# Performance work log

Hardware: AMD Instinct MI355X
Metric: run time of the kernel (lower is better)

Reference implementation:

```python
import jax, jax.numpy as jnp
import numpy as np

N = 10000          # num mesh vertices
NSPEC = 64         # spectral basis size (V[:, :64], D[:64, :])
K = 6              # Chebyshev order
IN_DESC = 352      # input descriptor dims (SHOT)
OUT_DESC = 256     # output descriptor dims
EPS = 1e-3


def _bn(x, g, b):
    # BatchNorm1d over the node (batch) dim, training-mode batch statistics
    m = x.mean(axis=0)
    v = x.var(axis=0)
    return (x - m) * jax.lax.rsqrt(v + EPS) * g + b


def _cheb(x, V, D, eigs, W, b):
    # Spectral Laplacian apply: L z = V @ (eigs * (D @ z)); cost O(N*64*C)
    def L(z):
        return V @ (eigs[:, None] * (D @ z))
    T_prev, T_cur = x, L(x)
    out = T_prev @ W[0] + T_cur @ W[1]
    for k in range(2, K):
        T_next = 2.0 * L(T_cur) - T_prev
        out = out + T_next @ W[k]
        T_prev, T_cur = T_cur, T_next
    return out + b


def setup_inputs() -> dict:
    key = jax.random.key(0)
    ks = jax.random.split(key, 12)
    s = lambda fan_in: 1.0 / np.sqrt(fan_in)
    return {
        "x": jax.random.normal(ks[0], (N, IN_DESC), jnp.float32),
        "V": jax.random.normal(ks[1], (N, NSPEC), jnp.float32) * (1.0 / np.sqrt(N)),
        "D": jax.random.normal(ks[2], (NSPEC, N), jnp.float32) * (1.0 / np.sqrt(N)),
        "eigs": jax.random.uniform(ks[3], (NSPEC,), jnp.float32),
        "fc1_w": jax.random.normal(ks[4], (IN_DESC, 64), jnp.float32) * s(IN_DESC),
        "fc1_b": jnp.zeros((64,), jnp.float32),
        "bf1_g": jnp.ones((64,), jnp.float32),
        "bf1_b": jnp.zeros((64,), jnp.float32),
        "W1": jax.random.normal(ks[5], (K, 64, 64), jnp.float32) * s(64 * K),
        "cb1": jnp.zeros((64,), jnp.float32),
        "b1_g": jnp.ones((64,), jnp.float32),
        "b1_b": jnp.zeros((64,), jnp.float32),
        "W2": jax.random.normal(ks[6], (K, 64, 64), jnp.float32) * s(64 * K),
        "cb2": jnp.zeros((64,), jnp.float32),
        "b2_g": jnp.ones((64,), jnp.float32),
        "b2_b": jnp.zeros((64,), jnp.float32),
        "W3": jax.random.normal(ks[7], (K, 64, 128), jnp.float32) * s(64 * K),
        "cb3": jnp.zeros((128,), jnp.float32),
        "b3_g": jnp.ones((128,), jnp.float32),
        "b3_b": jnp.zeros((128,), jnp.float32),
        "fc2_w": jax.random.normal(ks[8], (128, OUT_DESC), jnp.float32) * s(128),
        "fc2_b": jnp.zeros((OUT_DESC,), jnp.float32),
        "bf2_g": jnp.ones((OUT_DESC,), jnp.float32),
        "bf2_b": jnp.zeros((OUT_DESC,), jnp.float32),
        "fc3_w": jax.random.normal(ks[9], (OUT_DESC, N), jnp.float32) * s(OUT_DESC),
        "fc3_b": jnp.zeros((N,), jnp.float32),
    }


def reference(x, V, D, eigs, fc1_w, fc1_b, bf1_g, bf1_b,
              W1, cb1, b1_g, b1_b, W2, cb2, b2_g, b2_b,
              W3, cb3, b3_g, b3_b, fc2_w, fc2_b, bf2_g, bf2_b,
              fc3_w, fc3_b):
    h = jax.nn.relu(_bn(x @ fc1_w + fc1_b, bf1_g, bf1_b))
    h = jax.nn.relu(_bn(_cheb(h, V, D, eigs, W1, cb1), b1_g, b1_b))
    h = jax.nn.relu(_bn(_cheb(h, V, D, eigs, W2, cb2), b2_g, b2_b))
    h = jax.nn.relu(_bn(_cheb(h, V, D, eigs, W3, cb3), b3_g, b3_b))
    desc = jax.nn.relu(_bn(h @ fc2_w + fc2_b, bf2_g, bf2_b))
    logits = desc @ fc3_w + fc3_b  # [N, N] correspondence logits
    return jax.nn.log_softmax(logits, axis=1), desc
```

## Files before the change

kernel.cpp:

```cpp
#include <hip/hip_runtime.h>
#include <hip/hip_bf16.h>

#define NV 10000
#define PADM 10112

typedef __attribute__((ext_vector_type(8))) short bf16x8;
typedef __attribute__((ext_vector_type(4))) float f32x4;

__device__ __forceinline__ void g2l16(const void* g, void* l) {
  __builtin_amdgcn_global_load_lds((__attribute__((address_space(1))) void*)(void*)g,
                                   (__attribute__((address_space(3))) void*)l, 16, 0, 0);
}

__global__ __launch_bounds__(256) void gemm_f32(
    const float* __restrict__ A1, int K1, const float* __restrict__ A2, int K2,
    const float* __restrict__ B, const float* __restrict__ bias,
    float* __restrict__ Y, float* __restrict__ stats, int N)
{
  __shared__ float As[64][36];
  __shared__ float Bs[32][68];
  const int tid = threadIdx.x;
  const int row0 = blockIdx.x * 64;
  const int n0 = blockIdx.y * 64;
  const int tr = tid >> 4, tc = tid & 15;
  const int Ktot = K1 + K2;
  float acc[4][4];
#pragma unroll
  for (int i = 0; i < 4; ++i)
#pragma unroll
    for (int j = 0; j < 4; ++j) acc[i][j] = 0.f;

  for (int k0 = 0; k0 < Ktot; k0 += 32) {
    const float* Ap; int lda, ka;
    if (k0 < K1) { Ap = A1; lda = K1; ka = k0; }
    else         { Ap = A2; lda = K2; ka = k0 - K1; }
    __syncthreads();
    {
      int r = tid >> 3, seg = tid & 7;
#pragma unroll
      for (int h = 0; h < 2; ++h) {
        int rr = r + h * 32;
        int gr = row0 + rr; if (gr > NV - 1) gr = NV - 1;
        float4 v = *(const float4*)(Ap + (size_t)gr * lda + ka + seg * 4);
        *(float4*)&As[rr][seg * 4] = v;
      }
      int kr = tid >> 4, cseg = tid & 15;
#pragma unroll
      for (int h = 0; h < 2; ++h) {
        int kk = kr + h * 16;
        float4 v = *(const float4*)(B + (size_t)(k0 + kk) * N + n0 + cseg * 4);
        *(float4*)&Bs[kk][cseg * 4] = v;
      }
    }
    __syncthreads();
#pragma unroll 8
    for (int kk = 0; kk < 32; ++kk) {
      float4 bv = *(const float4*)&Bs[kk][tc * 4];
#pragma unroll
      for (int i = 0; i < 4; ++i) {
        float a = As[tr * 4 + i][kk];
        acc[i][0] = fmaf(a, bv.x, acc[i][0]);
        acc[i][1] = fmaf(a, bv.y, acc[i][1]);
        acc[i][2] = fmaf(a, bv.z, acc[i][2]);
        acc[i][3] = fmaf(a, bv.w, acc[i][3]);
      }
    }
  }
  float bvv[4];
#pragma unroll
  for (int j = 0; j < 4; ++j) bvv[j] = bias[n0 + tc * 4 + j];
  float cs[4] = {0.f, 0.f, 0.f, 0.f}, cq[4] = {0.f, 0.f, 0.f, 0.f};
#pragma unroll
  for (int i = 0; i < 4; ++i) {
    int gr = row0 + tr * 4 + i;
    bool ok = gr < NV;
    float o[4];
#pragma unroll
    for (int j = 0; j < 4; ++j) {
      float v = acc[i][j] + bvv[j];
      o[j] = v;
      if (ok) { cs[j] += v; cq[j] += v * v; }
    }
    if (ok) *(float4*)(Y + (size_t)gr * N + n0 + tc * 4) = make_float4(o[0], o[1], o[2], o[3]);
  }
  __syncthreads();
  float* red = &As[0][0];
#pragma unroll
  for (int j = 0; j < 4; ++j) {
    red[tr * 68 + tc * 4 + j] = cs[j];
    red[1088 + tr * 68 + tc * 4 + j] = cq[j];
  }
  __syncthreads();
  if (tid < 64) {
    float s = 0.f, q = 0.f;
#pragma unroll
    for (int t = 0; t < 16; ++t) { s += red[t * 68 + tid]; q += red[1088 + t * 68 + tid]; }
    atomicAdd(&stats[n0 + tid], s);
    atomicAdd(&stats[256 + n0 + tid], q);
  }
}

__global__ __launch_bounds__(256) void bn_relu(
    const float* __restrict__ Y, const float* __restrict__ stats,
    const float* __restrict__ g, const float* __restrict__ bt,
    float* __restrict__ out, unsigned short* __restrict__ outb, int C)
{
  int gid = blockIdx.x * 256 + threadIdx.x;
  int total = NV * (C >> 2);
  if (gid >= total) return;
  int c = (gid * 4) % C;
  float4 y = *(const float4*)(Y + (size_t)gid * 4);
  float vy[4] = {y.x, y.y, y.z, y.w};
  float o[4];
#pragma unroll
  for (int j = 0; j < 4; ++j) {
    int cc = c + j;
    float mean = stats[cc] * 1e-4f;
    float var  = stats[256 + cc] * 1e-4f - mean * mean;
    float sc = rsqrtf(var + 1e-3f) * g[cc];
    float sh = bt[cc] - mean * sc;
    o[j] = fmaxf(0.f, fmaf(vy[j], sc, sh));
  }
  *(float4*)(out + (size_t)gid * 4) = make_float4(o[0], o[1], o[2], o[3]);
  if (outb != nullptr) {
    unsigned short u[4];
#pragma unroll
    for (int j = 0; j < 4; ++j) {
      __hip_bfloat16 h = __float2bfloat16(o[j]);
      u[j] = *(unsigned short*)&h;
    }
    *(ushort2*)(outb + (size_t)gid * 4)     = make_ushort2(u[0], u[1]);
    *(ushort2*)(outb + (size_t)gid * 4 + 2) = make_ushort2(u[2], u[3]);
  }
}

__global__ __launch_bounds__(256) void dx_part(
    const float* __restrict__ Dm, const float* __restrict__ X, float* __restrict__ part)
{
  __shared__ float Ds[64][40];
  __shared__ float Xs[40][64];
  const int tid = threadIdx.x;
  const int k0 = blockIdx.x * 40;
  const float* xp = X + (size_t)k0 * 64;
  for (int i = tid; i < 2560; i += 256) ((float*)Xs)[i] = xp[i];
  {
    int r = tid >> 2, qq = tid & 3;
#pragma unroll
    for (int m = 0; m < 10; ++m) Ds[r][qq + 4 * m] = Dm[(size_t)r * NV + k0 + qq + 4 * m];
  }
  __syncthreads();
  const int j = tid & 63, ig = tid >> 6;
  float acc[16];
#pragma unroll
  for (int ii = 0; ii < 16; ++ii) acc[ii] = 0.f;
  for (int k = 0; k < 40; ++k) {
    float xv = Xs[k][j];
#pragma unroll
    for (int ii = 0; ii < 16; ++ii) acc[ii] = fmaf(Ds[ig * 16 + ii][k], xv, acc[ii]);
  }
  float* op = part + (size_t)blockIdx.x * 4096 + (size_t)ig * 1024 + j;
#pragma unroll
  for (int ii = 0; ii < 16; ++ii) op[ii * 64] = acc[ii];
}

__global__ __launch_bounds__(256) void dx_reduce(const float* __restrict__ part,
                                                 float* __restrict__ outm)
{
  int e = blockIdx.x * 256 + threadIdx.x;
  float s = 0.f;
  for (int b = 0; b < 250; ++b) s += part[(size_t)b * 4096 + e];
  outm[e] = s;
}

__global__ __launch_bounds__(256) void chainA(
    const float* __restrict__ DVm, const float* __restrict__ eigs, float* __restrict__ Acat)
{
  __shared__ float DVL[64][68];
  __shared__ float AL[3][64][68];
  __shared__ float ev[64];
  const int tid = threadIdx.x;
  for (int i = tid; i < 4096; i += 256) DVL[i >> 6][i & 63] = DVm[i];
  if (tid < 64) ev[tid] = eigs[tid];
  __syncthreads();
  for (int i = tid; i < 4096; i += 256) {
    int r = i >> 6, c = i & 63;
    AL[0][r][c] = 0.f;
    float v = (r == c) ? ev[r] : 0.f;
    AL[1][r][c] = v;
    Acat[i] = v;
  }
  __syncthreads();
  const int tr = tid >> 4, tc = tid & 15;
  float aK[4]; aK[0] = 0.f; aK[1] = -1.f; aK[2] = 0.f; aK[3] = 1.f;
  for (int k = 1; k <= 4; ++k) {
    int cur = k % 3, prv = (k - 1) % 3, nxt = (k + 1) % 3;
    float g4[4][4];
#pragma unroll
    for (int ii = 0; ii < 4; ++ii)
#pragma unroll
      for (int jj = 0; jj < 4; ++jj) g4[ii][jj] = 0.f;
    for (int p = 0; p < 64; ++p) {
      float4 av = *(const float4*)&AL[cur][p][tc * 4];
#pragma unroll
      for (int ii = 0; ii < 4; ++ii) {
        float dv = DVL[tr * 4 + ii][p];
        g4[ii][0] = fmaf(dv, av.x, g4[ii][0]);
        g4[ii][1] = fmaf(dv, av.y, g4[ii][1]);
        g4[ii][2] = fmaf(dv, av.z, g4[ii][2]);
        g4[ii][3] = fmaf(dv, av.w, g4[ii][3]);
      }
    }
    float ak = aK[k - 1];
#pragma unroll
    for (int ii = 0; ii < 4; ++ii) {
      int i = tr * 4 + ii;
#pragma unroll
      for (int jj = 0; jj < 4; ++jj) {
        int j = tc * 4 + jj;
        float gg = g4[ii][jj] + ((i == j) ? ak : 0.f);
        float v = 2.f * ev[i] * gg - AL[prv][i][j];
        AL[nxt][i][j] = v;
        Acat[(size_t)k * 4096 + i * 64 + j] = v;
      }
    }
    __syncthreads();
  }
}

__global__ __launch_bounds__(256) void mcat_k(
    const float* __restrict__ Acat, const float* __restrict__ S0, float* __restrict__ Mcat)
{
  __shared__ float AL[64][68];
  __shared__ float SL[64][68];
  const int kb = blockIdx.x;
  const int tid = threadIdx.x;
  for (int i = tid; i < 4096; i += 256) {
    AL[i >> 6][i & 63] = Acat[(size_t)kb * 4096 + i];
    SL[i >> 6][i & 63] = S0[i];
  }
  __syncthreads();
  const int tr = tid >> 4, tc = tid & 15;
  float g4[4][4];
#pragma unroll
  for (int ii = 0; ii < 4; ++ii)
#pragma unroll
    for (int jj = 0; jj < 4; ++jj) g4[ii][jj] = 0.f;
  for (int p = 0; p < 64; ++p) {
    float4 sv = *(const float4*)&SL[p][tc * 4];
#pragma unroll
    for (int ii = 0; ii < 4; ++ii) {
      float a = AL[tr * 4 + ii][p];
      g4[ii][0] = fmaf(a, sv.x, g4[ii][0]);
      g4[ii][1] = fmaf(a, sv.y, g4[ii][1]);
      g4[ii][2] = fmaf(a, sv.z, g4[ii][2]);
      g4[ii][3] = fmaf(a, sv.w, g4[ii][3]);
    }
  }
#pragma unroll
  for (int ii = 0; ii < 4; ++ii)
#pragma unroll
    for (int jj = 0; jj < 4; ++jj)
      Mcat[(size_t)(tr * 4 + ii) * 320 + kb * 64 + tc * 4 + jj] = g4[ii][jj];
}

__global__ __launch_bounds__(256) void bc_k(
    const float* __restrict__ W, const float* __restrict__ Mcat,
    float* __restrict__ Bc, int Cout)
{
  int e = blockIdx.x * 256 + threadIdx.x;
  int row = e / Cout, j = e - row * Cout;
  if (row < 64) {
    Bc[e] = W[row * Cout + j] - W[128 * Cout + row * Cout + j] + W[256 * Cout + row * Cout + j];
  } else {
    int i = row - 64;
    const float* wc = W + 64 * Cout + j;
    const float* mr = Mcat + (size_t)i * 320;
    float s = 0.f;
#pragma unroll 8
    for (int qq = 0; qq < 320; ++qq) s = fmaf(mr[qq], wc[(size_t)qq * Cout], s);
    Bc[e] = s;
  }
}

__global__ __launch_bounds__(256) void cast_transpose_w(
    const float* __restrict__ w, unsigned short* __restrict__ wT)
{
  __shared__ float tile[32][33];
  int n0 = blockIdx.x * 32, k0 = blockIdx.y * 32;
  int t = threadIdx.x;
  int rr = t >> 5, cc = t & 31;
#pragma unroll
  for (int p = 0; p < 4; ++p) {
    int k = k0 + rr + p * 8, n = n0 + cc;
    tile[rr + p * 8][cc] = (n < NV) ? w[(size_t)k * NV + n] : 0.f;
  }
  __syncthreads();
#pragma unroll
  for (int p = 0; p < 4; ++p) {
    int n = n0 + rr + p * 8, k = k0 + cc;
    __hip_bfloat16 h = __float2bfloat16(tile[cc][rr + p * 8]);
    wT[(size_t)n * 256 + k] = *(unsigned short*)&h;
  }
}

__global__ __launch_bounds__(256) void fc3_gemm(
    const unsigned short* __restrict__ A, const unsigned short* __restrict__ Bt,
    const float* __restrict__ bias, float* __restrict__ out, float* __restrict__ rowsum)
{
  __shared__ unsigned short As[128 * 64];
  __shared__ unsigned short Bs[128 * 64];
  const int tid = threadIdx.x;
  const int wv = tid >> 6, lane = tid & 63;
  const int row0 = blockIdx.x * 128, col0 = blockIdx.y * 128;
  const int wr = wv >> 1, wc = wv & 1;
  f32x4 acc[4][4];
#pragma unroll
  for (int i = 0; i < 4; ++i)
#pragma unroll
    for (int j = 0; j < 4; ++j)
#pragma unroll
      for (int e = 0; e < 4; ++e) acc[i][j][e] = 0.f;

  const int rs = wv * 8 + (lane >> 3);
  const int csg = (lane & 7) * 8;
  for (int k0 = 0; k0 < 256; k0 += 64) {
    __syncthreads();
#pragma unroll
    for (int i = 0; i < 4; ++i) {
      g2l16(A  + (size_t)(row0 + i * 32 + rs) * 256 + k0 + csg, &As[(i * 32 + rs) * 64 + csg]);
      g2l16(Bt + (size_t)(col0 + i * 32 + rs) * 256 + k0 + csg, &Bs[(i * 32 + rs) * 64 + csg]);
    }
    asm volatile("s_waitcnt vmcnt(0)" ::: "memory");
    __syncthreads();
    const int mbase = wr * 64 + (lane & 15);
    const int nbase = wc * 64 + (lane & 15);
#pragma unroll
    for (int kk = 0; kk < 2; ++kk) {
      const int kb = kk * 32 + (lane >> 4) * 8;
      bf16x8 af[4], bf[4];
#pragma unroll
      for (int mi = 0; mi < 4; ++mi) af[mi] = *(const bf16x8*)&As[(mbase + mi * 16) * 64 + kb];
#pragma unroll
      for (int ni = 0; ni < 4; ++ni) bf[ni] = *(const bf16x8*)&Bs[(nbase + ni * 16) * 64 + kb];
#pragma unroll
      for (int mi = 0; mi < 4; ++mi)
#pragma unroll
        for (int ni = 0; ni < 4; ++ni)
          acc[mi][ni] = __builtin_amdgcn_mfma_f32_16x16x32_bf16(af[mi], bf[ni], acc[mi][ni], 0, 0, 0);
    }
  }
  const int q = lane >> 4, cl = lane & 15;
#pragma unroll
  for (int mi = 0; mi < 4; ++mi) {
#pragma unroll
    for (int r = 0; r < 4; ++r) {
      int grow = row0 + wr * 64 + mi * 16 + q * 4 + r;
      float ps = 0.f;
#pragma unroll
      for (int ni = 0; ni < 4; ++ni) {
        int gcol = col0 + wc * 64 + ni * 16 + cl;
        if (gcol < NV) {
          float v = acc[mi][ni][r] + bias[gcol];
          if (grow < NV) {
            out[(size_t)grow * NV + gcol] = v;
            ps += __expf(v - 20.f);
          }
        }
      }
#pragma unroll
      for (int s = 1; s < 16; s <<= 1) ps += __shfl_xor(ps, s, 64);
      if (cl == 0 && grow < NV) atomicAdd(&rowsum[grow], ps);
    }
  }
}

__global__ __launch_bounds__(256) void norm_lsm(float* __restrict__ out,
                                                const float* __restrict__ rowsum)
{
  int c4 = blockIdx.x * 256 + threadIdx.x;
  if (c4 >= 2500) return;
  int row = blockIdx.y;
  float l = 20.f + __logf(rowsum[row]);
  float4* p = (float4*)(out + (size_t)row * NV + (size_t)c4 * 4);
  float4 v = *p;
  v.x -= l; v.y -= l; v.z -= l; v.w -= l;
  *p = v;
}

extern "C" void kernel_launch(void* const* d_in, const int* in_sizes, int n_in,
                              void* d_out, int out_size, void* d_ws, size_t ws_size,
                              hipStream_t stream)
{
  const float* x     = (const float*)d_in[0];
  const float* V     = (const float*)d_in[1];
  const float* D     = (const float*)d_in[2];
  const float* eigs  = (const float*)d_in[3];
  const float* fc1_w = (const float*)d_in[4];
  const float* fc1_b = (const float*)d_in[5];
  const float* bf1_g = (const float*)d_in[6];
  const float* bf1_b = (const float*)d_in[7];
  const float* W1    = (const float*)d_in[8];
  const float* cb1   = (const float*)d_in[9];
  const float* b1_g  = (const float*)d_in[10];
  const float* b1_b  = (const float*)d_in[11];
  const float* W2    = (const float*)d_in[12];
  const float* cb2   = (const float*)d_in[13];
  const float* b2_g  = (const float*)d_in[14];
  const float* b2_b  = (const float*)d_in[15];
  const float* W3    = (const float*)d_in[16];
  const float* cb3   = (const float*)d_in[17];
  const float* b3_g  = (const float*)d_in[18];
  const float* b3_b  = (const float*)d_in[19];
  const float* fc2_w = (const float*)d_in[20];
  const float* fc2_b = (const float*)d_in[21];
  const float* bf2_g = (const float*)d_in[22];
  const float* bf2_b = (const float*)d_in[23];
  const float* fc3_w = (const float*)d_in[24];
  const float* fc3_b = (const float*)d_in[25];
  (void)in_sizes; (void)n_in; (void)out_size;

  float* ws = (float*)d_ws;
  float* rowsum = ws;
  float* stats  = ws + 10000;
  float* DVm    = ws + 22560;
  float* Acat   = ws + 26656;
  float* S0     = ws + 47136;
  float* Mcat   = ws + 51232;
  float* Bc     = ws + 71712;
  float* part   = ws + 88096;
  float* Ybuf   = ws + 1112096;
  float* actA   = ws + 3672096;
  float* actB   = ws + 4312096;
  float* h3     = ws + 4952096;
  unsigned short* descb = (unsigned short*)(ws + 6232096);
  unsigned short* wT    = (unsigned short*)(ws + 7526432);
  if (ws_size < (size_t)8820768 * 4) return;

  float* out_lsm  = (float*)d_out;
  float* out_desc = out_lsm + (size_t)100000000;

  hipMemsetAsync(ws, 0, 12560 * sizeof(float), stream);
  hipMemsetAsync(descb + (size_t)NV * 256, 0, (size_t)(PADM - NV) * 256 * 2, stream);

  cast_transpose_w<<<dim3(316, 8), 256, 0, stream>>>(fc3_w, wT);

  dx_part<<<250, 256, 0, stream>>>(D, V, part);
  dx_reduce<<<16, 256, 0, stream>>>(part, DVm);
  chainA<<<1, 256, 0, stream>>>(DVm, eigs, Acat);

  gemm_f32<<<dim3(157, 1), 256, 0, stream>>>(x, 352, nullptr, 0, fc1_w, fc1_b,
                                             Ybuf, stats + 0 * 512, 64);
  bn_relu<<<625, 256, 0, stream>>>(Ybuf, stats + 0 * 512, bf1_g, bf1_b, actA, nullptr, 64);

  dx_part<<<250, 256, 0, stream>>>(D, actA, part);
  dx_reduce<<<16, 256, 0, stream>>>(part, S0);
  mcat_k<<<5, 256, 0, stream>>>(Acat, S0, Mcat);
  bc_k<<<32, 256, 0, stream>>>(W1, Mcat, Bc, 64);
  gemm_f32<<<dim3(157, 1), 256, 0, stream>>>(actA, 64, V, 64, Bc, cb1,
                                             Ybuf, stats + 1 * 512, 64);
  bn_relu<<<625, 256, 0, stream>>>(Ybuf, stats + 1 * 512, b1_g, b1_b, actB, nullptr, 64);

  dx_part<<<250, 256, 0, stream>>>(D, actB, part);
  dx_reduce<<<16, 256, 0, stream>>>(part, S0);
  mcat_k<<<5, 256, 0, stream>>>(Acat, S0, Mcat);
  bc_k<<<32, 256, 0, stream>>>(W2, Mcat, Bc, 64);
  gemm_f32<<<dim3(157, 1), 256, 0, stream>>>(actB, 64, V, 64, Bc, cb2,
                                             Ybuf, stats + 2 * 512, 64);
  bn_relu<<<625, 256, 0, stream>>>(Ybuf, stats + 2 * 512, b2_g, b2_b, actA, nullptr, 64);

  dx_part<<<250, 256, 0, stream>>>(D, actA, part);
  dx_reduce<<<16, 256, 0, stream>>>(part, S0);
  mcat_k<<<5, 256, 0, stream>>>(Acat, S0, Mcat);
  bc_k<<<64, 256, 0, stream>>>(W3, Mcat, Bc, 128);
  gemm_f32<<<dim3(157, 2), 256, 0, stream>>>(actA, 64, V, 64, Bc, cb3,
                                             Ybuf, stats + 3 * 512, 128);
  bn_relu<<<1250, 256, 0, stream>>>(Ybuf, stats + 3 * 512, b3_g, b3_b, h3, nullptr, 128);

  gemm_f32<<<dim3(157, 4), 256, 0, stream>>>(h3, 128, nullptr, 0, fc2_w, fc2_b,
                                             Ybuf, stats + 4 * 512, 256);
  bn_relu<<<2500, 256, 0, stream>>>(Ybuf, stats + 4 * 512, bf2_g, bf2_b,
                                    out_desc, descb, 256);

  fc3_gemm<<<dim3(79, 79), 256, 0, stream>>>(descb, wT, fc3_b, out_lsm, rowsum);
  norm_lsm<<<dim3(10, NV), 256, 0, stream>>>(out_lsm, rowsum);
}
```

Before: 1.051 ms.

## Recompute fc3 GEMM to write normalized log-softmax once; atomic D@X reduction

The fc3 logits GEMM now runs twice. The first pass only accumulates row sums of exp, and the second recomputes the tile and writes logits minus the log-normalizer directly. This removes the write-then-read-modify-write of the 400MB output in a separate normalization kernel, at the cost of doubling the bf16 MFMA work. The D@X partial-sum reduction kernels are also replaced by atomicAdd into per-layer zeroed buffers, which drops a kernel launch and the partial-buffer traffic per layer.

```diff
diff --git a/kernel.cpp b/kernel.cpp
--- a/kernel.cpp
+++ b/kernel.cpp
@@ -134,8 +134,8 @@
   }
 }
 
-__global__ __launch_bounds__(256) void dx_part(
-    const float* __restrict__ Dm, const float* __restrict__ X, float* __restrict__ part)
+__global__ __launch_bounds__(256) void dx_atomic(
+    const float* __restrict__ Dm, const float* __restrict__ X, float* __restrict__ outm)
 {
   __shared__ float Ds[64][40];
   __shared__ float Xs[40][64];
@@ -158,18 +158,9 @@
 #pragma unroll
     for (int ii = 0; ii < 16; ++ii) acc[ii] = fmaf(Ds[ig * 16 + ii][k], xv, acc[ii]);
   }
-  float* op = part + (size_t)blockIdx.x * 4096 + (size_t)ig * 1024 + j;
-#pragma unroll
-  for (int ii = 0; ii < 16; ++ii) op[ii * 64] = acc[ii];
-}
-
-__global__ __launch_bounds__(256) void dx_reduce(const float* __restrict__ part,
-                                                 float* __restrict__ outm)
-{
-  int e = blockIdx.x * 256 + threadIdx.x;
-  float s = 0.f;
-  for (int b = 0; b < 250; ++b) s += part[(size_t)b * 4096 + e];
-  outm[e] = s;
+  float* op = outm + (size_t)ig * 1024 + j;
+#pragma unroll
+  for (int ii = 0; ii < 16; ++ii) atomicAdd(&op[ii * 64], acc[ii]);
 }
 
 __global__ __launch_bounds__(256) void chainA(
@@ -303,9 +294,9 @@
   }
 }
 
-__global__ __launch_bounds__(256) void fc3_gemm(
+__global__ __launch_bounds__(256) void fc3_rowsum(
     const unsigned short* __restrict__ A, const unsigned short* __restrict__ Bt,
-    const float* __restrict__ bias, float* __restrict__ out, float* __restrict__ rowsum)
+    const float* __restrict__ bias, float* __restrict__ rowsum)
 {
   __shared__ unsigned short As[128 * 64];
   __shared__ unsigned short Bs[128 * 64];
@@ -356,15 +347,11 @@
     for (int r = 0; r < 4; ++r) {
       int grow = row0 + wr * 64 + mi * 16 + q * 4 + r;
       float ps = 0.f;
-#pragma unroll
-      for (int ni = 0; ni < 4; ++ni) {
-        int gcol = col0 + wc * 64 + ni * 16 + cl;
-        if (gcol < NV) {
-          float v = acc[mi][ni][r] + bias[gcol];
-          if (grow < NV) {
-            out[(size_t)grow * NV + gcol] = v;
-            ps += __expf(v - 20.f);
-          }
+      if (grow < NV) {
+#pragma unroll
+        for (int ni = 0; ni < 4; ++ni) {
+          int gcol = col0 + wc * 64 + ni * 16 + cl;
+          if (gcol < NV) ps += __expf(acc[mi][ni][r] + bias[gcol] - 20.f);
         }
       }
 #pragma unroll
@@ -374,17 +361,70 @@
   }
 }
 
-__global__ __launch_bounds__(256) void norm_lsm(float* __restrict__ out,
-                                                const float* __restrict__ rowsum)
-{
-  int c4 = blockIdx.x * 256 + threadIdx.x;
-  if (c4 >= 2500) return;
-  int row = blockIdx.y;
-  float l = 20.f + __logf(rowsum[row]);
-  float4* p = (float4*)(out + (size_t)row * NV + (size_t)c4 * 4);
-  float4 v = *p;
-  v.x -= l; v.y -= l; v.z -= l; v.w -= l;
-  *p = v;
+__global__ __launch_bounds__(256) void fc3_write(
+    const unsigned short* __restrict__ A, const unsigned short* __restrict__ Bt,
+    const float* __restrict__ bias, const float* __restrict__ rowsum,
+    float* __restrict__ out)
+{
+  __shared__ unsigned short As[128 * 64];
+  __shared__ unsigned short Bs[128 * 64];
+  const int tid = threadIdx.x;
+  const int wv = tid >> 6, lane = tid & 63;
+  const int row0 = blockIdx.x * 128, col0 = blockIdx.y * 128;
+  const int wr = wv >> 1, wc = wv & 1;
+  f32x4 acc[4][4];
+#pragma unroll
+  for (int i = 0; i < 4; ++i)
+#pragma unroll
+    for (int j = 0; j < 4; ++j)
+#pragma unroll
+      for (int e = 0; e < 4; ++e) acc[i][j][e] = 0.f;
+
+  const int rs = wv * 8 + (lane >> 3);
+  const int csg = (lane & 7) * 8;
+  for (int k0 = 0; k0 < 256; k0 += 64) {
+    __syncthreads();
+#pragma unroll
+    for (int i = 0; i < 4; ++i) {
+      g2l16(A  + (size_t)(row0 + i * 32 + rs) * 256 + k0 + csg, &As[(i * 32 + rs) * 64 + csg]);
+      g2l16(Bt + (size_t)(col0 + i * 32 + rs) * 256 + k0 + csg, &Bs[(i * 32 + rs) * 64 + csg]);
+    }
+    asm volatile("s_waitcnt vmcnt(0)" ::: "memory");
+    __syncthreads();
+    const int mbase = wr * 64 + (lane & 15);
+    const int nbase = wc * 64 + (lane & 15);
+#pragma unroll
+    for (int kk = 0; kk < 2; ++kk) {
+      const int kb = kk * 32 + (lane >> 4) * 8;
+      bf16x8 af[4], bf[4];
+#pragma unroll
+      for (int mi = 0; mi < 4; ++mi) af[mi] = *(const bf16x8*)&As[(mbase + mi * 16) * 64 + kb];
+#pragma unroll
+      for (int ni = 0; ni < 4; ++ni) bf[ni] = *(const bf16x8*)&Bs[(nbase + ni * 16) * 64 + kb];
+#pragma unroll
+      for (int mi = 0; mi < 4; ++mi)
+#pragma unroll
+        for (int ni = 0; ni < 4; ++ni)
+          acc[mi][ni] = __builtin_amdgcn_mfma_f32_16x16x32_bf16(af[mi], bf[ni], acc[mi][ni], 0, 0, 0);
+    }
+  }
+  const int q = lane >> 4, cl = lane & 15;
+#pragma unroll
+  for (int mi = 0; mi < 4; ++mi) {
+#pragma unroll
+    for (int r = 0; r < 4; ++r) {
+      int grow = row0 + wr * 64 + mi * 16 + q * 4 + r;
+      if (grow < NV) {
+        float l = 20.f + __logf(rowsum[grow]);
+#pragma unroll
+        for (int ni = 0; ni < 4; ++ni) {
+          int gcol = col0 + wc * 64 + ni * 16 + cl;
+          if (gcol < NV)
+            out[(size_t)grow * NV + gcol] = acc[mi][ni][r] + bias[gcol] - l;
+        }
+      }
+    }
+  }
 }
 
 extern "C" void kernel_launch(void* const* d_in, const int* in_sizes, int n_in,
@@ -422,55 +462,52 @@
   float* ws = (float*)d_ws;
   float* rowsum = ws;
   float* stats  = ws + 10000;
-  float* DVm    = ws + 22560;
-  float* Acat   = ws + 26656;
-  float* S0     = ws + 47136;
-  float* Mcat   = ws + 51232;
-  float* Bc     = ws + 71712;
-  float* part   = ws + 88096;
-  float* Ybuf   = ws + 1112096;
-  float* actA   = ws + 3672096;
-  float* actB   = ws + 4312096;
-  float* h3     = ws + 4952096;
-  unsigned short* descb = (unsigned short*)(ws + 6232096);
-  unsigned short* wT    = (unsigned short*)(ws + 7526432);
-  if (ws_size < (size_t)8820768 * 4) return;
+  float* DVm    = ws + 12560;
+  float* S0a    = ws + 16656;
+  float* S0b    = ws + 20752;
+  float* S0c    = ws + 24848;
+  float* Acat   = ws + 28944;
+  float* Mcat   = ws + 49424;
+  float* Bc     = ws + 69904;
+  float* Ybuf   = ws + 86288;
+  float* actA   = ws + 2646288;
+  float* actB   = ws + 3286288;
+  float* h3     = ws + 3926288;
+  unsigned short* descb = (unsigned short*)(ws + 5206288);
+  unsigned short* wT    = (unsigned short*)(ws + 6500624);
+  if (ws_size < (size_t)7794960 * 4) return;
 
   float* out_lsm  = (float*)d_out;
   float* out_desc = out_lsm + (size_t)100000000;
 
-  hipMemsetAsync(ws, 0, 12560 * sizeof(float), stream);
+  hipMemsetAsync(ws, 0, 28944 * sizeof(float), stream);
   hipMemsetAsync(descb + (size_t)NV * 256, 0, (size_t)(PADM - NV) * 256 * 2, stream);
 
   cast_transpose_w<<<dim3(316, 8), 256, 0, stream>>>(fc3_w, wT);
 
-  dx_part<<<250, 256, 0, stream>>>(D, V, part);
-  dx_reduce<<<16, 256, 0, stream>>>(part, DVm);
+  dx_atomic<<<250, 256, 0, stream>>>(D, V, DVm);
   chainA<<<1, 256, 0, stream>>>(DVm, eigs, Acat);
 
   gemm_f32<<<dim3(157, 1), 256, 0, stream>>>(x, 352, nullptr, 0, fc1_w, fc1_b,
                                              Ybuf, stats + 0 * 512, 64);
   bn_relu<<<625, 256, 0, stream>>>(Ybuf, stats + 0 * 512, bf1_g, bf1_b, actA, nullptr, 64);
 
-  dx_part<<<250, 256, 0, stream>>>(D, actA, part);
-  dx_reduce<<<16, 256, 0, stream>>>(part, S0);
-  mcat_k<<<5, 256, 0, stream>>>(Acat, S0, Mcat);
+  dx_atomic<<<250, 256, 0, stream>>>(D, actA, S0a);
+  mcat_k<<<5, 256, 0, stream>>>(Acat, S0a, Mcat);
   bc_k<<<32, 256, 0, stream>>>(W1, Mcat, Bc, 64);
   gemm_f32<<<dim3(157, 1), 256, 0, stream>>>(actA, 64, V, 64, Bc, cb1,
                                              Ybuf, stats + 1 * 512, 64);
   bn_relu<<<625, 256, 0, stream>>>(Ybuf, stats + 1 * 512, b1_g, b1_b, actB, nullptr, 64);
 
-  dx_part<<<250, 256, 0, stream>>>(D, actB, part);
-  dx_reduce<<<16, 256, 0, stream>>>(part, S0);
-  mcat_k<<<5, 256, 0, stream>>>(Acat, S0, Mcat);
+  dx_atomic<<<250, 256, 0, stream>>>(D, actB, S0b);
+  mcat_k<<<5, 256, 0, stream>>>(Acat, S0b, Mcat);
   bc_k<<<32, 256, 0, stream>>>(W2, Mcat, Bc, 64);
   gemm_f32<<<dim3(157, 1), 256, 0, stream>>>(actB, 64, V, 64, Bc, cb2,
                                              Ybuf, stats + 2 * 512, 64);
   bn_relu<<<625, 256, 0, stream>>>(Ybuf, stats + 2 * 512, b2_g, b2_b, actA, nullptr, 64);
 
-  dx_part<<<250, 256, 0, stream>>>(D, actA, part);
-  dx_reduce<<<16, 256, 0, stream>>>(part, S0);
-  mcat_k<<<5, 256, 0, stream>>>(Acat, S0, Mcat);
+  dx_atomic<<<250, 256, 0, stream>>>(D, actA, S0c);
+  mcat_k<<<5, 256, 0, stream>>>(Acat, S0c, Mcat);
   bc_k<<<64, 256, 0, stream>>>(W3, Mcat, Bc, 128);
   gemm_f32<<<dim3(157, 2), 256, 0, stream>>>(actA, 64, V, 64, Bc, cb3,
                                              Ybuf, stats + 3 * 512, 128);
@@ -481,6 +518,6 @@
   bn_relu<<<2500, 256, 0, stream>>>(Ybuf, stats + 4 * 512, bf2_g, bf2_b,
                                     out_desc, descb, 256);
 
-  fc3_gemm<<<dim3(79, 79), 256, 0, stream>>>(descb, wT, fc3_b, out_lsm, rowsum);
-  norm_lsm<<<dim3(10, NV), 256, 0, stream>>>(out_lsm, rowsum);
-}
+  fc3_rowsum<<<dim3(79, 79), 256, 0, stream>>>(descb, wT, fc3_b, rowsum);
+  fc3_write<<<dim3(79, 79), 256, 0, stream>>>(descb, wT, fc3_b, rowsum, out_lsm);
+}
```

Result: slower. 1.074 ms (+2.2%).
